# Optimization experiments

Hardware: AMD Instinct MI355X
Metric: run time of the kernel (lower is better)

## Reference

```python
import jax, jax.numpy as jnp
import numpy as np

NUM_GRAPHS = 2048


def gcn_conv(x, W, b, edge, N):
    # PyG GCNConv: x' = D^{-1/2} (A + I) D^{-1/2} (x W) + b
    src, dst = edge[0], edge[1]
    loop = jnp.arange(N, dtype=src.dtype)
    src = jnp.concatenate([src, loop])
    dst = jnp.concatenate([dst, loop])
    h = x @ W  # [N, out]
    deg = jax.ops.segment_sum(jnp.ones(dst.shape, x.dtype), dst, num_segments=N)
    dinv = jnp.where(deg > 0, jax.lax.rsqrt(deg), 0.0)
    norm = dinv[src] * dinv[dst]  # [E+N]
    out = jax.ops.segment_sum(h[src] * norm[:, None], dst, num_segments=N)
    return out + b


def pool_max_mean(x, batch, G):
    mx = jax.ops.segment_max(x, batch, num_segments=G)
    mx = jnp.where(jnp.isfinite(mx), mx, 0.0)  # guard empty segments
    s = jax.ops.segment_sum(x, batch, num_segments=G)
    cnt = jax.ops.segment_sum(jnp.ones((x.shape[0],), x.dtype), batch, num_segments=G)
    mean = s / jnp.maximum(cnt, 1.0)[:, None]
    return mx, mean


def setup_inputs() -> dict:
    key = jax.random.key(0)
    ks = jax.random.split(key, 20)
    F, CE, SE, DD = 64, 64, 32, 128
    Nc, Ec, Ns, Es = 100000, 1250000, 100000, 1250000

    def glorot(k, shape):
        fan_in, fan_out = shape[0], shape[1]
        lim = np.sqrt(6.0 / (fan_in + fan_out)).astype(np.float32)
        return jax.random.uniform(k, shape, jnp.float32, -lim, lim)

    inp = {
        "c": jax.random.normal(ks[0], (Nc, F), jnp.float32),
        "c_edge": jax.random.randint(ks[1], (2, Ec), 0, Nc),
        "c_batch": jnp.sort(jax.random.randint(ks[2], (Nc,), 0, NUM_GRAPHS)),
        "s": jax.random.normal(ks[3], (Ns, F), jnp.float32),
        "s_edge": jax.random.randint(ks[4], (2, Es), 0, Ns),
        "s_batch": jnp.sort(jax.random.randint(ks[5], (Ns,), 0, NUM_GRAPHS)),
        "Wc0": glorot(ks[6], (F, CE)), "bc0": jnp.zeros((CE,), jnp.float32),
        "Wc1": glorot(ks[7], (CE, CE)), "bc1": jnp.zeros((CE,), jnp.float32),
        "Wc2": glorot(ks[8], (CE, CE)), "bc2": jnp.zeros((CE,), jnp.float32),
        "Ws0": glorot(ks[9], (F, SE)), "bs0": jnp.zeros((SE,), jnp.float32),
        "Ws1": glorot(ks[10], (SE, SE)), "bs1": jnp.zeros((SE,), jnp.float32),
        "Ws2": glorot(ks[11], (SE, SE)), "bs2": jnp.zeros((SE,), jnp.float32),
        "Wd": glorot(ks[12], ((CE + SE) * 2, DD)), "bd": jnp.zeros((DD,), jnp.float32),
        "Wo": glorot(ks[13], (DD, 1)), "bo": jnp.zeros((1,), jnp.float32),
    }
    return inp


def reference(c, c_edge, c_batch, s, s_edge, s_batch,
              Wc0, bc0, Wc1, bc1, Wc2, bc2,
              Ws0, bs0, Ws1, bs1, Ws2, bs2,
              Wd, bd, Wo, bo):
    Nc, Ns = c.shape[0], s.shape[0]
    cro = jax.nn.relu(gcn_conv(c, Wc0, bc0, c_edge, Nc))
    cro = jax.nn.relu(gcn_conv(cro, Wc1, bc1, c_edge, Nc))
    cro = jax.nn.relu(gcn_conv(cro, Wc2, bc2, c_edge, Nc))
    solv = jax.nn.relu(gcn_conv(s, Ws0, bs0, s_edge, Ns))
    solv = jax.nn.relu(gcn_conv(solv, Ws1, bs1, s_edge, Ns))
    solv = jax.nn.relu(gcn_conv(solv, Ws2, bs2, s_edge, Ns))
    c_mx, c_mean = pool_max_mean(cro, c_batch, NUM_GRAPHS)
    s_mx, s_mean = pool_max_mean(solv, s_batch, NUM_GRAPHS)
    embed = jnp.concatenate([c_mx, c_mean, s_mx, s_mean], axis=1)  # [G, 192]
    dense = jax.nn.relu(embed @ Wd + bd)
    out = dense @ Wo + bo  # [G, 1]
    return out, embed
```

## Files before the change

kernel.cpp:

```cpp
#include <hip/hip_runtime.h>
#include <hip/hip_fp16.h>
#include <math.h>


static inline int cdiv(int a, int b) { return (a + b - 1) / b; }

#define BUCKET_CAP 8192
#define P1_CHUNK   4096

typedef _Float16 v8h __attribute__((ext_vector_type(8)));
typedef float    v4f __attribute__((ext_vector_type(4)));

__global__ void zero_int(int* __restrict__ p, int n) {
    int i = blockIdx.x * blockDim.x + threadIdx.x;
    if (i < n) p[i] = 0;
}

__global__ __launch_bounds__(256) void p1_partition(const int* __restrict__ c_edge, int Ec,
                                                    const int* __restrict__ s_edge, int Es,
                                                    int Nc_pad, int Etot, int nbuck,
                                                    int* __restrict__ bucket_fill,
                                                    unsigned* __restrict__ pk) {
    __shared__ unsigned       wbuf[P1_CHUNK];
    __shared__ unsigned short bbuf[P1_CHUNK];
    __shared__ int            hist[512];
    int e0 = blockIdx.x * P1_CHUNK;
    int n  = Etot - e0;
    if (n > P1_CHUNK) n = P1_CHUNK;
    for (int i = threadIdx.x; i < nbuck; i += 256) hist[i] = 0;
    __syncthreads();
    for (int i = threadIdx.x; i < n; i += 256) {
        int e = e0 + i, src, g;
        if (e < Ec) { src = c_edge[e]; g = c_edge[Ec + e]; }
        else        { int e2 = e - Ec; src = s_edge[e2]; g = Nc_pad + s_edge[Es + e2]; }
        int b   = g >> 9;
        wbuf[i] = ((unsigned)(g & 511) << 17) | (unsigned)src;
        bbuf[i] = (unsigned short)b;
        atomicAdd(&hist[b], 1);
    }
    __syncthreads();
    for (int i = threadIdx.x; i < nbuck; i += 256) {
        int h = hist[i];
        hist[i] = h ? atomicAdd(&bucket_fill[i], h) : 0;
    }
    __syncthreads();
    for (int i = threadIdx.x; i < n; i += 256) {
        int b    = bbuf[i];
        int slot = atomicAdd(&hist[b], 1);
        if (slot < BUCKET_CAP) pk[(size_t)b * BUCKET_CAP + slot] = wbuf[i];
    }
}

__global__ __launch_bounds__(512) void p2_scanbuckets(const int* __restrict__ fill, int nbuck,
                                                      int* __restrict__ basearr,
                                                      int* __restrict__ off_all, int Ntot_pad, int Etot) {
    __shared__ int sh[512];
    int v = (threadIdx.x < nbuck) ? fill[threadIdx.x] : 0;
    sh[threadIdx.x] = v;
    __syncthreads();
    for (int ofs = 1; ofs < 512; ofs <<= 1) {
        int t = (threadIdx.x >= ofs) ? sh[threadIdx.x - ofs] : 0;
        __syncthreads();
        sh[threadIdx.x] += t;
        __syncthreads();
    }
    if (threadIdx.x < nbuck) basearr[threadIdx.x] = sh[threadIdx.x] - v;
    if (threadIdx.x == 0) off_all[Ntot_pad] = Etot;
}

__global__ __launch_bounds__(512) void p3_build(const unsigned* __restrict__ pk,
                                                const int* __restrict__ fillarr,
                                                const int* __restrict__ basearr,
                                                int* __restrict__ off_all,
                                                float* __restrict__ dinv,
                                                int* __restrict__ csr) {
    __shared__ int sh[512];
    int b    = blockIdx.x;
    int fill = fillarr[b];
    if (fill > BUCKET_CAP) fill = BUCKET_CAP;
    int base = basearr[b];
    const unsigned* reg = pk + (size_t)b * BUCKET_CAP;
    sh[threadIdx.x] = 0;
    __syncthreads();
    for (int i = threadIdx.x; i < fill; i += 512) atomicAdd(&sh[reg[i] >> 17], 1);
    __syncthreads();
    int cnt = sh[threadIdx.x];
    for (int ofs = 1; ofs < 512; ofs <<= 1) {
        int t = (threadIdx.x >= ofs) ? sh[threadIdx.x - ofs] : 0;
        __syncthreads();
        sh[threadIdx.x] += t;
        __syncthreads();
    }
    int excl = sh[threadIdx.x] - cnt;
    int node = b * 512 + threadIdx.x;
    off_all[node] = base + excl;
    dinv[node]    = rsqrtf((float)(cnt + 1));
    __syncthreads();
    sh[threadIdx.x] = excl;
    __syncthreads();
    for (int i = threadIdx.x; i < fill; i += 512) {
        unsigned w    = reg[i];
        int      slot = atomicAdd(&sh[w >> 17], 1);
        csr[base + slot] = (int)(w & 0x1FFFFu);
    }
}

template <int K, int M, typename TIN>
__device__ void gemm_mfma(int bid, const TIN* __restrict__ X, const float* __restrict__ W,
                          const float* __restrict__ dinv, __half* __restrict__ H, int N,
                          char* smem_) {
    constexpr int RB = 64;
    constexpr int KP = K + 8;
    constexpr int NT = M / 16;
    constexpr int KS = K / 32;
    _Float16* Xh = (_Float16*)smem_;
    _Float16* Wz = Xh + RB * KP;
    const int t    = threadIdx.x;
    const int row0 = bid * RB;

    constexpr int WENT = NT * KS * 64;
    for (int idx = t; idx < WENT; idx += 256) {
        int lane = idx & 63, rest = idx >> 6;
        int ks = rest % KS, ntl = rest / KS;
        int kbase = ks * 32 + (lane >> 4) * 8;
        int col   = ntl * 16 + (lane & 15);
        union { float4 f4; _Float16 h[8]; } u;
#pragma unroll
        for (int j = 0; j < 8; ++j) u.h[j] = (_Float16)W[(kbase + j) * M + col];
        *(float4*)(Wz + idx * 8) = u.f4;
    }
    if constexpr (sizeof(TIN) == 4) {
        constexpr int NI = RB * K / 4;
        for (int idx = t; idx < NI; idx += 256) {
            int row = idx / (K / 4), k4 = idx % (K / 4);
            int gr = row0 + row;
            float4 v = make_float4(0.f, 0.f, 0.f, 0.f);
            if (gr < N) v = *(const float4*)((const float*)X + (size_t)gr * K + k4 * 4);
            union { float2 f2; _Float16 h[4]; } u;
            u.h[0] = (_Float16)v.x; u.h[1] = (_Float16)v.y;
            u.h[2] = (_Float16)v.z; u.h[3] = (_Float16)v.w;
            *(float2*)(Xh + row * KP + k4 * 4) = u.f2;
        }
    } else {
        constexpr int NI = RB * K / 8;
        for (int idx = t; idx < NI; idx += 256) {
            int row = idx / (K / 8), k8 = idx % (K / 8);
            int gr = row0 + row;
            float4 v = make_float4(0.f, 0.f, 0.f, 0.f);
            if (gr < N) v = *(const float4*)((const __half*)X + (size_t)gr * K + k8 * 8);
            *(float4*)(Xh + row * KP + k8 * 8) = v;
        }
    }
    __syncthreads();

    const int wave = t >> 6, lane = t & 63;
    const int quad = lane >> 4, nl = lane & 15;
    const int rowA = wave * 16 + nl;

    v4f acc[NT];
#pragma unroll
    for (int i = 0; i < NT; ++i) acc[i] = (v4f){0.f, 0.f, 0.f, 0.f};

#pragma unroll
    for (int ks = 0; ks < KS; ++ks) {
        v8h a = *(const v8h*)(Xh + rowA * KP + ks * 32 + quad * 8);
#pragma unroll
        for (int ntl = 0; ntl < NT; ++ntl) {
            v8h b = *(const v8h*)(Wz + ((ntl * KS + ks) * 64 + lane) * 8);
            acc[ntl] = __builtin_amdgcn_mfma_f32_16x16x32_f16(a, b, acc[ntl], 0, 0, 0);
        }
    }

#pragma unroll
    for (int r = 0; r < 4; ++r) {
        int gr = row0 + wave * 16 + quad * 4 + r;
        if (gr < N) {
            float dv = dinv[gr];
#pragma unroll
            for (int ntl = 0; ntl < NT; ++ntl)
                H[(size_t)gr * M + ntl * 16 + nl] = __float2half(acc[ntl][r] * dv);
        }
    }
}

__device__ __forceinline__ float4 load4h(const float2* __restrict__ base, size_t idx) {
    float2 r = base[idx];
    union { float2 f2; __half2 h2[2]; } u;
    u.f2 = r;
    float2 a = __half22float2(u.h2[0]);
    float2 b = __half22float2(u.h2[1]);
    return make_float4(a.x, a.y, b.x, b.y);
}

template <int M>
__device__ void agg_body(int bid, const __half* __restrict__ H,
                         const int* __restrict__ off_g,
                         const int* __restrict__ csr,
                         const float* __restrict__ dinv_g,
                         const float* __restrict__ b,
                         __half* __restrict__ out, int Nloc) {
    constexpr int L   = M / 4;
    constexpr int NPW = 64 / L;
    int lane = threadIdx.x & 63;
    int wave = threadIdx.x >> 6;
    int fq   = lane & (L - 1);
    int sub  = lane / L;
    int node = (bid * 4 + wave) * NPW + sub;
    if (node >= Nloc) return;
    const float2* H4 = (const float2*)H;
    int j0 = off_g[node], j1 = off_g[node + 1];
    float4 acc = load4h(H4, (size_t)node * L + fq);
    int j = j0;
    for (; j + 8 <= j1; j += 8) {
        int s0 = csr[j],     s1 = csr[j + 1], s2 = csr[j + 2], s3 = csr[j + 3];
        int s4 = csr[j + 4], s5 = csr[j + 5], s6 = csr[j + 6], s7 = csr[j + 7];
        float4 a0 = load4h(H4, (size_t)s0 * L + fq);
        float4 a1 = load4h(H4, (size_t)s1 * L + fq);
        float4 a2 = load4h(H4, (size_t)s2 * L + fq);
        float4 a3 = load4h(H4, (size_t)s3 * L + fq);
        float4 a4 = load4h(H4, (size_t)s4 * L + fq);
        float4 a5 = load4h(H4, (size_t)s5 * L + fq);
        float4 a6 = load4h(H4, (size_t)s6 * L + fq);
        float4 a7 = load4h(H4, (size_t)s7 * L + fq);
        acc.x += (a0.x + a1.x + a2.x + a3.x) + (a4.x + a5.x + a6.x + a7.x);
        acc.y += (a0.y + a1.y + a2.y + a3.y) + (a4.y + a5.y + a6.y + a7.y);
        acc.z += (a0.z + a1.z + a2.z + a3.z) + (a4.z + a5.z + a6.z + a7.z);
        acc.w += (a0.w + a1.w + a2.w + a3.w) + (a4.w + a5.w + a6.w + a7.w);
    }
    for (; j + 4 <= j1; j += 4) {
        int s0 = csr[j], s1 = csr[j + 1], s2 = csr[j + 2], s3 = csr[j + 3];
        float4 a0 = load4h(H4, (size_t)s0 * L + fq);
        float4 a1 = load4h(H4, (size_t)s1 * L + fq);
        float4 a2 = load4h(H4, (size_t)s2 * L + fq);
        float4 a3 = load4h(H4, (size_t)s3 * L + fq);
        acc.x += a0.x + a1.x + a2.x + a3.x;
        acc.y += a0.y + a1.y + a2.y + a3.y;
        acc.z += a0.z + a1.z + a2.z + a3.z;
        acc.w += a0.w + a1.w + a2.w + a3.w;
    }
    for (; j < j1; ++j) {
        float4 a = load4h(H4, (size_t)csr[j] * L + fq);
        acc.x += a.x; acc.y += a.y; acc.z += a.z; acc.w += a.w;
    }
    float  dv = dinv_g[node];
    float4 bb = ((const float4*)b)[fq];
    float  vx = dv * acc.x + bb.x;
    float  vy = dv * acc.y + bb.y;
    float  vz = dv * acc.z + bb.z;
    float  vw = dv * acc.w + bb.w;
    union { float2 f2; __half2 h2[2]; } o;
    o.h2[0] = __floats2half2_rn(vx > 0.f ? vx : 0.f, vy > 0.f ? vy : 0.f);
    o.h2[1] = __floats2half2_rn(vz > 0.f ? vz : 0.f, vw > 0.f ? vw : 0.f);
    ((float2*)out)[(size_t)node * L + fq] = o.f2;
}

__global__ __launch_bounds__(256) void gemmBoth0(const float* __restrict__ Xc, const float* __restrict__ Wc,
                                                 __half* __restrict__ cH, int Nc,
                                                 const float* __restrict__ Xs, const float* __restrict__ Ws,
                                                 __half* __restrict__ sH, int Ns,
                                                 const float* __restrict__ dinv_all, int Nc_pad, int nbC) {
    __shared__ __align__(16) char smem[17408];
    if (blockIdx.x < nbC) gemm_mfma<64, 64, float>(blockIdx.x, Xc, Wc, dinv_all, cH, Nc, smem);
    else                  gemm_mfma<64, 32, float>(blockIdx.x - nbC, Xs, Ws, dinv_all + Nc_pad, sH, Ns, smem);
}

__global__ __launch_bounds__(256) void gemmBoth(const __half* __restrict__ Xc, const float* __restrict__ Wc,
                                                __half* __restrict__ cH, int Nc,
                                                const __half* __restrict__ Xs, const float* __restrict__ Ws,
                                                __half* __restrict__ sH, int Ns,
                                                const float* __restrict__ dinv_all, int Nc_pad, int nbC) {
    __shared__ __align__(16) char smem[17408];
    if (blockIdx.x < nbC) gemm_mfma<64, 64, __half>(blockIdx.x, Xc, Wc, dinv_all, cH, Nc, smem);
    else                  gemm_mfma<32, 32, __half>(blockIdx.x - nbC, Xs, Ws, dinv_all + Nc_pad, sH, Ns, smem);
}

__global__ __launch_bounds__(256) void aggBoth(const __half* __restrict__ cH, const __half* __restrict__ sH,
                                               const int* __restrict__ off_all, const int* __restrict__ csr_all,
                                               const float* __restrict__ dinv_all,
                                               const float* __restrict__ bc, const float* __restrict__ bs,
                                               __half* __restrict__ outc, __half* __restrict__ outs,
                                               int Nc, int Ns, int Nc_pad, int nbC) {
    if (blockIdx.x < nbC)
        agg_body<64>(blockIdx.x, cH, off_all, csr_all, dinv_all, bc, outc, Nc);
    else
        agg_body<32>(blockIdx.x - nbC, sH, off_all + Nc_pad, csr_all,
                     dinv_all + Nc_pad, bs, outs, Ns);
}

__device__ __forceinline__ int lbound(const int* __restrict__ a, int n, int key) {
    int lo = 0, hi = n;
    while (lo < hi) {
        int mid = (lo + hi) >> 1;
        if (a[mid] < key) lo = mid + 1; else hi = mid;
    }
    return lo;
}

__global__ __launch_bounds__(128) void poolDense(const __half* __restrict__ cX, const int* __restrict__ c_batch, int Nc,
                                                 const __half* __restrict__ sX, const int* __restrict__ s_batch, int Ns,
                                                 const float* __restrict__ Wd, const float* __restrict__ bd,
                                                 const float* __restrict__ Wo, const float* __restrict__ bo,
                                                 float* __restrict__ outv, float* __restrict__ embed) {
    __shared__ float e[192];
    __shared__ float red[128];
    int g = blockIdx.x, t = threadIdx.x;
    if (t < 64) {
        int lo = lbound(c_batch, Nc, g), hi = lbound(c_batch, Nc, g + 1);
        float mx = 0.f, sm = 0.f;
        for (int i = lo; i < hi; ++i) {
            float v = __half2float(cX[(size_t)i * 64 + t]);
            mx = fmaxf(mx, v); sm += v;
        }
        int cn = hi - lo;
        e[t]      = mx;
        e[64 + t] = sm / (float)(cn > 0 ? cn : 1);
    } else if (t < 96) {
        int f  = t - 64;
        int lo = lbound(s_batch, Ns, g), hi = lbound(s_batch, Ns, g + 1);
        float mx = 0.f, sm = 0.f;
        for (int i = lo; i < hi; ++i) {
            float v = __half2float(sX[(size_t)i * 32 + f]);
            mx = fmaxf(mx, v); sm += v;
        }
        int cn = hi - lo;
        e[128 + f] = mx;
        e[160 + f] = sm / (float)(cn > 0 ? cn : 1);
    }
    __syncthreads();
    for (int k = t; k < 192; k += 128) embed[(size_t)g * 192 + k] = e[k];
    float acc = bd[t];
    for (int k = 0; k < 192; ++k) acc += e[k] * Wd[k * 128 + t];
    float d = acc > 0.f ? acc : 0.f;
    red[t]  = d * Wo[t];
    __syncthreads();
    for (int ofs = 64; ofs > 0; ofs >>= 1) {
        if (t < ofs) red[t] += red[t + ofs];
        __syncthreads();
    }
    if (t == 0) outv[g] = red[0] + bo[0];
}


extern "C" void kernel_launch(void* const* d_in, const int* in_sizes, int n_in,
                              void* d_out, int out_size, void* d_ws, size_t ws_size,
                              hipStream_t stream) {
    const float* c       = (const float*)d_in[0];
    const int*   c_edge  = (const int*)d_in[1];
    const int*   c_batch = (const int*)d_in[2];
    const float* s       = (const float*)d_in[3];
    const int*   s_edge  = (const int*)d_in[4];
    const int*   s_batch = (const int*)d_in[5];
    const float* Wc0 = (const float*)d_in[6],  *bc0 = (const float*)d_in[7];
    const float* Wc1 = (const float*)d_in[8],  *bc1 = (const float*)d_in[9];
    const float* Wc2 = (const float*)d_in[10], *bc2 = (const float*)d_in[11];
    const float* Ws0 = (const float*)d_in[12], *bs0 = (const float*)d_in[13];
    const float* Ws1 = (const float*)d_in[14], *bs1 = (const float*)d_in[15];
    const float* Ws2 = (const float*)d_in[16], *bs2 = (const float*)d_in[17];
    const float* Wd  = (const float*)d_in[18], *bd  = (const float*)d_in[19];
    const float* Wo  = (const float*)d_in[20], *bo  = (const float*)d_in[21];

    const int Nc = in_sizes[0] / 64;
    const int Ec = in_sizes[1] / 2;
    const int Ns = in_sizes[3] / 64;
    const int Es = in_sizes[4] / 2;
    const int G  = out_size / 193;
    const int Nc_pad   = cdiv(Nc, 512) * 512;
    const int Ns_pad   = cdiv(Ns, 512) * 512;
    const int Ntot_pad = Nc_pad + Ns_pad;
    const int Etot     = Ec + Es;
    const int nbuck    = Ntot_pad >> 9;

    char* p = (char*)d_ws;
    auto  alloc = [&](size_t bytes) -> void* {
        void* r = (void*)p;
        p += (bytes + 255) & ~(size_t)255;
        return r;
    };
    int*      bucket_fill = (int*)alloc(512 * 4);
    int*      bucket_base = (int*)alloc(512 * 4);
    unsigned* pk          = (unsigned*)alloc((size_t)nbuck * BUCKET_CAP * 4);
    int*      off_all     = (int*)alloc(((size_t)Ntot_pad + 1) * 4);
    int*      csr_all     = (int*)alloc((size_t)Etot * 4);
    float*    dinv_all    = (float*)alloc((size_t)Ntot_pad * 4);
    __half*   bufC        = (__half*)alloc((size_t)Nc * 64 * 2);
    __half*   bufS        = (__half*)alloc((size_t)Ns * 32 * 2);
    __half*   cH          = (__half*)alloc((size_t)Nc * 64 * 2);
    __half*   sH          = (__half*)alloc((size_t)Ns * 32 * 2);

    float* outv  = (float*)d_out;
    float* embed = outv + G;

    const int nbGmC = cdiv(Nc, 64), nbGmS = cdiv(Ns, 64);
    const int nbAgC = Nc_pad / 16,  nbAgS = Ns_pad / 32;

    zero_int<<<cdiv(nbuck, 256), 256, 0, stream>>>(bucket_fill, nbuck);
    p1_partition<<<cdiv(Etot, P1_CHUNK), 256, 0, stream>>>(c_edge, Ec, s_edge, Es,
                                                           Nc_pad, Etot, nbuck, bucket_fill, pk);
    p2_scanbuckets<<<1, 512, 0, stream>>>(bucket_fill, nbuck, bucket_base, off_all, Ntot_pad, Etot);
    p3_build<<<nbuck, 512, 0, stream>>>(pk, bucket_fill, bucket_base,
                                        off_all, dinv_all, csr_all);

    gemmBoth0<<<nbGmC + nbGmS, 256, 0, stream>>>(c, Wc0, cH, Nc, s, Ws0, sH, Ns,
                                                 dinv_all, Nc_pad, nbGmC);
    aggBoth<<<nbAgC + nbAgS, 256, 0, stream>>>(cH, sH, off_all, csr_all, dinv_all,
                                               bc0, bs0, bufC, bufS, Nc, Ns, Nc_pad, nbAgC);
    gemmBoth<<<nbGmC + nbGmS, 256, 0, stream>>>(bufC, Wc1, cH, Nc, bufS, Ws1, sH, Ns,
                                                dinv_all, Nc_pad, nbGmC);
    aggBoth<<<nbAgC + nbAgS, 256, 0, stream>>>(cH, sH, off_all, csr_all, dinv_all,
                                               bc1, bs1, bufC, bufS, Nc, Ns, Nc_pad, nbAgC);
    gemmBoth<<<nbGmC + nbGmS, 256, 0, stream>>>(bufC, Wc2, cH, Nc, bufS, Ws2, sH, Ns,
                                                dinv_all, Nc_pad, nbGmC);
    aggBoth<<<nbAgC + nbAgS, 256, 0, stream>>>(cH, sH, off_all, csr_all, dinv_all,
                                               bc2, bs2, bufC, bufS, Nc, Ns, Nc_pad, nbAgC);

    poolDense<<<G, 128, 0, stream>>>(bufC, c_batch, Nc, bufS, s_batch, Ns,
                                     Wd, bd, Wo, bo, outv, embed);
}
```

Measured before the change: 367.6 us.

## Fuse GCN aggregation with next layer's MFMA GEMM via shared memory

New measurement: 370.1 us. No clear change (+0.7%).

```diff
diff --git a/kernel.cpp b/kernel.cpp
--- a/kernel.cpp
+++ b/kernel.cpp
@@ -105,84 +105,6 @@
     }
 }
 
-template <int K, int M, typename TIN>
-__device__ void gemm_mfma(int bid, const TIN* __restrict__ X, const float* __restrict__ W,
-                          const float* __restrict__ dinv, __half* __restrict__ H, int N,
-                          char* smem_) {
-    constexpr int RB = 64;
-    constexpr int KP = K + 8;
-    constexpr int NT = M / 16;
-    constexpr int KS = K / 32;
-    _Float16* Xh = (_Float16*)smem_;
-    _Float16* Wz = Xh + RB * KP;
-    const int t    = threadIdx.x;
-    const int row0 = bid * RB;
-
-    constexpr int WENT = NT * KS * 64;
-    for (int idx = t; idx < WENT; idx += 256) {
-        int lane = idx & 63, rest = idx >> 6;
-        int ks = rest % KS, ntl = rest / KS;
-        int kbase = ks * 32 + (lane >> 4) * 8;
-        int col   = ntl * 16 + (lane & 15);
-        union { float4 f4; _Float16 h[8]; } u;
-#pragma unroll
-        for (int j = 0; j < 8; ++j) u.h[j] = (_Float16)W[(kbase + j) * M + col];
-        *(float4*)(Wz + idx * 8) = u.f4;
-    }
-    if constexpr (sizeof(TIN) == 4) {
-        constexpr int NI = RB * K / 4;
-        for (int idx = t; idx < NI; idx += 256) {
-            int row = idx / (K / 4), k4 = idx % (K / 4);
-            int gr = row0 + row;
-            float4 v = make_float4(0.f, 0.f, 0.f, 0.f);
-            if (gr < N) v = *(const float4*)((const float*)X + (size_t)gr * K + k4 * 4);
-            union { float2 f2; _Float16 h[4]; } u;
-            u.h[0] = (_Float16)v.x; u.h[1] = (_Float16)v.y;
-            u.h[2] = (_Float16)v.z; u.h[3] = (_Float16)v.w;
-            *(float2*)(Xh + row * KP + k4 * 4) = u.f2;
-        }
-    } else {
-        constexpr int NI = RB * K / 8;
-        for (int idx = t; idx < NI; idx += 256) {
-            int row = idx / (K / 8), k8 = idx % (K / 8);
-            int gr = row0 + row;
-            float4 v = make_float4(0.f, 0.f, 0.f, 0.f);
-            if (gr < N) v = *(const float4*)((const __half*)X + (size_t)gr * K + k8 * 8);
-            *(float4*)(Xh + row * KP + k8 * 8) = v;
-        }
-    }
-    __syncthreads();
-
-    const int wave = t >> 6, lane = t & 63;
-    const int quad = lane >> 4, nl = lane & 15;
-    const int rowA = wave * 16 + nl;
-
-    v4f acc[NT];
-#pragma unroll
-    for (int i = 0; i < NT; ++i) acc[i] = (v4f){0.f, 0.f, 0.f, 0.f};
-
-#pragma unroll
-    for (int ks = 0; ks < KS; ++ks) {
-        v8h a = *(const v8h*)(Xh + rowA * KP + ks * 32 + quad * 8);
-#pragma unroll
-        for (int ntl = 0; ntl < NT; ++ntl) {
-            v8h b = *(const v8h*)(Wz + ((ntl * KS + ks) * 64 + lane) * 8);
-            acc[ntl] = __builtin_amdgcn_mfma_f32_16x16x32_f16(a, b, acc[ntl], 0, 0, 0);
-        }
-    }
-
-#pragma unroll
-    for (int r = 0; r < 4; ++r) {
-        int gr = row0 + wave * 16 + quad * 4 + r;
-        if (gr < N) {
-            float dv = dinv[gr];
-#pragma unroll
-            for (int ntl = 0; ntl < NT; ++ntl)
-                H[(size_t)gr * M + ntl * 16 + nl] = __float2half(acc[ntl][r] * dv);
-        }
-    }
-}
-
 __device__ __forceinline__ float4 load4h(const float2* __restrict__ base, size_t idx) {
     float2 r = base[idx];
     union { float2 f2; __half2 h2[2]; } u;
@@ -192,24 +114,9 @@
     return make_float4(a.x, a.y, b.x, b.y);
 }
 
-template <int M>
-__device__ void agg_body(int bid, const __half* __restrict__ H,
-                         const int* __restrict__ off_g,
-                         const int* __restrict__ csr,
-                         const float* __restrict__ dinv_g,
-                         const float* __restrict__ b,
-                         __half* __restrict__ out, int Nloc) {
-    constexpr int L   = M / 4;
-    constexpr int NPW = 64 / L;
-    int lane = threadIdx.x & 63;
-    int wave = threadIdx.x >> 6;
-    int fq   = lane & (L - 1);
-    int sub  = lane / L;
-    int node = (bid * 4 + wave) * NPW + sub;
-    if (node >= Nloc) return;
-    const float2* H4 = (const float2*)H;
-    int j0 = off_g[node], j1 = off_g[node + 1];
-    float4 acc = load4h(H4, (size_t)node * L + fq);
+__device__ __forceinline__ void gather_acc(const float2* __restrict__ H4, int L, int fq,
+                                           const int* __restrict__ csr, int j0, int j1,
+                                           float4& acc) {
     int j = j0;
     for (; j + 8 <= j1; j += 8) {
         int s0 = csr[j],     s1 = csr[j + 1], s2 = csr[j + 2], s3 = csr[j + 3];
@@ -242,6 +149,174 @@
         float4 a = load4h(H4, (size_t)csr[j] * L + fq);
         acc.x += a.x; acc.y += a.y; acc.z += a.z; acc.w += a.w;
     }
+}
+
+template <int K, int M, typename TIN>
+__device__ void gemm_mfma(int bid, const TIN* __restrict__ X, const float* __restrict__ W,
+                          const float* __restrict__ dinv, __half* __restrict__ H, int N,
+                          char* smem_) {
+    constexpr int RB = 64, KP = K + 8, NT = M / 16, KS = K / 32;
+    _Float16* Xh = (_Float16*)smem_;
+    _Float16* Wz = Xh + RB * KP;
+    const int t    = threadIdx.x;
+    const int row0 = bid * RB;
+
+    constexpr int WENT = NT * KS * 64;
+    for (int idx = t; idx < WENT; idx += 256) {
+        int lane = idx & 63, rest = idx >> 6;
+        int ks = rest % KS, ntl = rest / KS;
+        int kbase = ks * 32 + (lane >> 4) * 8;
+        int col   = ntl * 16 + (lane & 15);
+        union { float4 f4; _Float16 h[8]; } u;
+#pragma unroll
+        for (int j = 0; j < 8; ++j) u.h[j] = (_Float16)W[(kbase + j) * M + col];
+        *(float4*)(Wz + idx * 8) = u.f4;
+    }
+    if constexpr (sizeof(TIN) == 4) {
+        constexpr int NI = RB * K / 4;
+        for (int idx = t; idx < NI; idx += 256) {
+            int row = idx / (K / 4), k4 = idx % (K / 4);
+            int gr = row0 + row;
+            float4 v = make_float4(0.f, 0.f, 0.f, 0.f);
+            if (gr < N) v = *(const float4*)((const float*)X + (size_t)gr * K + k4 * 4);
+            union { float2 f2; _Float16 h[4]; } u;
+            u.h[0] = (_Float16)v.x; u.h[1] = (_Float16)v.y;
+            u.h[2] = (_Float16)v.z; u.h[3] = (_Float16)v.w;
+            *(float2*)(Xh + row * KP + k4 * 4) = u.f2;
+        }
+    } else {
+        constexpr int NI = RB * K / 8;
+        for (int idx = t; idx < NI; idx += 256) {
+            int row = idx / (K / 8), k8 = idx % (K / 8);
+            int gr = row0 + row;
+            float4 v = make_float4(0.f, 0.f, 0.f, 0.f);
+            if (gr < N) v = *(const float4*)((const __half*)X + (size_t)gr * K + k8 * 8);
+            *(float4*)(Xh + row * KP + k8 * 8) = v;
+        }
+    }
+    __syncthreads();
+
+    const int wave = t >> 6, lane = t & 63;
+    const int quad = lane >> 4, nl = lane & 15;
+    const int rowA = wave * 16 + nl;
+
+    v4f acc[NT];
+#pragma unroll
+    for (int i = 0; i < NT; ++i) acc[i] = (v4f){0.f, 0.f, 0.f, 0.f};
+#pragma unroll
+    for (int ks = 0; ks < KS; ++ks) {
+        v8h a = *(const v8h*)(Xh + rowA * KP + ks * 32 + quad * 8);
+#pragma unroll
+        for (int ntl = 0; ntl < NT; ++ntl) {
+            v8h b = *(const v8h*)(Wz + ((ntl * KS + ks) * 64 + lane) * 8);
+            acc[ntl] = __builtin_amdgcn_mfma_f32_16x16x32_f16(a, b, acc[ntl], 0, 0, 0);
+        }
+    }
+#pragma unroll
+    for (int r = 0; r < 4; ++r) {
+        int gr = row0 + wave * 16 + quad * 4 + r;
+        if (gr < N) {
+            float dv = dinv[gr];
+#pragma unroll
+            for (int ntl = 0; ntl < NT; ++ntl)
+                H[(size_t)gr * M + ntl * 16 + nl] = __float2half(acc[ntl][r] * dv);
+        }
+    }
+}
+
+template <int M>
+__device__ void aggGemm_body(int bid, const __half* __restrict__ Hin,
+                             const int* __restrict__ off_g, const int* __restrict__ csr,
+                             const float* __restrict__ dinv_g, const float* __restrict__ bvec,
+                             const float* __restrict__ Wnext, __half* __restrict__ Hout,
+                             int Nloc, char* smem_) {
+    constexpr int KP = M + 8, NT = M / 16, KS = M / 32;
+    constexpr int L = M / 4, NPW = 64 / L, ROUNDS = 64 / (4 * NPW);
+    _Float16* Xh = (_Float16*)smem_;
+    _Float16* Wz = Xh + 64 * KP;
+    const int t = threadIdx.x;
+    const int row0 = bid * 64;
+    const int lane = t & 63, wave = t >> 6;
+
+    constexpr int WENT = NT * KS * 64;
+    for (int idx = t; idx < WENT; idx += 256) {
+        int ln = idx & 63, rest = idx >> 6;
+        int ks = rest % KS, ntl = rest / KS;
+        int kbase = ks * 32 + (ln >> 4) * 8;
+        int col   = ntl * 16 + (ln & 15);
+        union { float4 f4; _Float16 h[8]; } u;
+#pragma unroll
+        for (int j = 0; j < 8; ++j) u.h[j] = (_Float16)Wnext[(kbase + j) * M + col];
+        *(float4*)(Wz + idx * 8) = u.f4;
+    }
+
+    const int fq = lane & (L - 1), sub = lane / L;
+    const float2* H4 = (const float2*)Hin;
+#pragma unroll
+    for (int r = 0; r < ROUNDS; ++r) {
+        int local = r * (4 * NPW) + wave * NPW + sub;
+        int node  = row0 + local;
+        float4 acc = make_float4(0.f, 0.f, 0.f, 0.f);
+        if (node < Nloc) {
+            int j0 = off_g[node], j1 = off_g[node + 1];
+            acc = load4h(H4, (size_t)node * L + fq);
+            gather_acc(H4, L, fq, csr, j0, j1, acc);
+            float  dv = dinv_g[node];
+            float4 bb = ((const float4*)bvec)[fq];
+            acc.x = fmaxf(dv * acc.x + bb.x, 0.f);
+            acc.y = fmaxf(dv * acc.y + bb.y, 0.f);
+            acc.z = fmaxf(dv * acc.z + bb.z, 0.f);
+            acc.w = fmaxf(dv * acc.w + bb.w, 0.f);
+        }
+        union { float2 f2; __half2 hh[2]; } o;
+        o.hh[0] = __floats2half2_rn(acc.x, acc.y);
+        o.hh[1] = __floats2half2_rn(acc.z, acc.w);
+        *(float2*)(Xh + local * KP + 4 * fq) = o.f2;
+    }
+    __syncthreads();
+
+    const int quad = lane >> 4, nl = lane & 15;
+    const int rowA = wave * 16 + nl;
+    v4f acc2[NT];
+#pragma unroll
+    for (int i = 0; i < NT; ++i) acc2[i] = (v4f){0.f, 0.f, 0.f, 0.f};
+#pragma unroll
+    for (int ks = 0; ks < KS; ++ks) {
+        v8h a = *(const v8h*)(Xh + rowA * KP + ks * 32 + quad * 8);
+#pragma unroll
+        for (int ntl = 0; ntl < NT; ++ntl) {
+            v8h b = *(const v8h*)(Wz + ((ntl * KS + ks) * 64 + lane) * 8);
+            acc2[ntl] = __builtin_amdgcn_mfma_f32_16x16x32_f16(a, b, acc2[ntl], 0, 0, 0);
+        }
+    }
+#pragma unroll
+    for (int r = 0; r < 4; ++r) {
+        int gr = row0 + wave * 16 + quad * 4 + r;
+        if (gr < Nloc) {
+            float dv = dinv_g[gr];
+#pragma unroll
+            for (int ntl = 0; ntl < NT; ++ntl)
+                Hout[(size_t)gr * M + ntl * 16 + nl] = __float2half(acc2[ntl][r] * dv);
+        }
+    }
+}
+
+template <int M>
+__device__ void agg_body(int bid, const __half* __restrict__ H,
+                         const int* __restrict__ off_g, const int* __restrict__ csr,
+                         const float* __restrict__ dinv_g, const float* __restrict__ b,
+                         __half* __restrict__ out, int Nloc) {
+    constexpr int L = M / 4, NPW = 64 / L;
+    int lane = threadIdx.x & 63;
+    int wave = threadIdx.x >> 6;
+    int fq   = lane & (L - 1);
+    int sub  = lane / L;
+    int node = (bid * 4 + wave) * NPW + sub;
+    if (node >= Nloc) return;
+    const float2* H4 = (const float2*)H;
+    int j0 = off_g[node], j1 = off_g[node + 1];
+    float4 acc = load4h(H4, (size_t)node * L + fq);
+    gather_acc(H4, L, fq, csr, j0, j1, acc);
     float  dv = dinv_g[node];
     float4 bb = ((const float4*)b)[fq];
     float  vx = dv * acc.x + bb.x;
@@ -264,14 +339,19 @@
     else                  gemm_mfma<64, 32, float>(blockIdx.x - nbC, Xs, Ws, dinv_all + Nc_pad, sH, Ns, smem);
 }
 
-__global__ __launch_bounds__(256) void gemmBoth(const __half* __restrict__ Xc, const float* __restrict__ Wc,
-                                                __half* __restrict__ cH, int Nc,
-                                                const __half* __restrict__ Xs, const float* __restrict__ Ws,
-                                                __half* __restrict__ sH, int Ns,
-                                                const float* __restrict__ dinv_all, int Nc_pad, int nbC) {
+__global__ __launch_bounds__(256) void aggGemmBoth(const __half* __restrict__ cHin, __half* __restrict__ cHout,
+                                                   const __half* __restrict__ sHin, __half* __restrict__ sHout,
+                                                   const int* __restrict__ off_all, const int* __restrict__ csr_all,
+                                                   const float* __restrict__ dinv_all,
+                                                   const float* __restrict__ bc, const float* __restrict__ bs,
+                                                   const float* __restrict__ Wc, const float* __restrict__ Ws,
+                                                   int Nc, int Ns, int Nc_pad, int nbC) {
     __shared__ __align__(16) char smem[17408];
-    if (blockIdx.x < nbC) gemm_mfma<64, 64, __half>(blockIdx.x, Xc, Wc, dinv_all, cH, Nc, smem);
-    else                  gemm_mfma<32, 32, __half>(blockIdx.x - nbC, Xs, Ws, dinv_all + Nc_pad, sH, Ns, smem);
+    if (blockIdx.x < nbC)
+        aggGemm_body<64>(blockIdx.x, cHin, off_all, csr_all, dinv_all, bc, Wc, cHout, Nc, smem);
+    else
+        aggGemm_body<32>(blockIdx.x - nbC, sHin, off_all + Nc_pad, csr_all,
+                         dinv_all + Nc_pad, bs, Ws, sHout, Ns, smem);
 }
 
 __global__ __launch_bounds__(256) void aggBoth(const __half* __restrict__ cH, const __half* __restrict__ sH,
@@ -384,13 +464,16 @@
     float*    dinv_all    = (float*)alloc((size_t)Ntot_pad * 4);
     __half*   bufC        = (__half*)alloc((size_t)Nc * 64 * 2);
     __half*   bufS        = (__half*)alloc((size_t)Ns * 32 * 2);
-    __half*   cH          = (__half*)alloc((size_t)Nc * 64 * 2);
-    __half*   sH          = (__half*)alloc((size_t)Ns * 32 * 2);
+    __half*   cHa         = (__half*)alloc((size_t)Nc * 64 * 2);
+    __half*   sHa         = (__half*)alloc((size_t)Ns * 32 * 2);
+    __half*   cHb         = (__half*)alloc((size_t)Nc * 64 * 2);
+    __half*   sHb         = (__half*)alloc((size_t)Ns * 32 * 2);
 
     float* outv  = (float*)d_out;
     float* embed = outv + G;
 
     const int nbGmC = cdiv(Nc, 64), nbGmS = cdiv(Ns, 64);
+    const int nbFzC = Nc_pad / 64,  nbFzS = Ns_pad / 64;
     const int nbAgC = Nc_pad / 16,  nbAgS = Ns_pad / 32;
 
     zero_int<<<cdiv(nbuck, 256), 256, 0, stream>>>(bucket_fill, nbuck);
@@ -400,17 +483,15 @@
     p3_build<<<nbuck, 512, 0, stream>>>(pk, bucket_fill, bucket_base,
                                         off_all, dinv_all, csr_all);
 
-    gemmBoth0<<<nbGmC + nbGmS, 256, 0, stream>>>(c, Wc0, cH, Nc, s, Ws0, sH, Ns,
+    gemmBoth0<<<nbGmC + nbGmS, 256, 0, stream>>>(c, Wc0, cHa, Nc, s, Ws0, sHa, Ns,
                                                  dinv_all, Nc_pad, nbGmC);
-    aggBoth<<<nbAgC + nbAgS, 256, 0, stream>>>(cH, sH, off_all, csr_all, dinv_all,
-                                               bc0, bs0, bufC, bufS, Nc, Ns, Nc_pad, nbAgC);
-    gemmBoth<<<nbGmC + nbGmS, 256, 0, stream>>>(bufC, Wc1, cH, Nc, bufS, Ws1, sH, Ns,
-                                                dinv_all, Nc_pad, nbGmC);
-    aggBoth<<<nbAgC + nbAgS, 256, 0, stream>>>(cH, sH, off_all, csr_all, dinv_all,
-                                               bc1, bs1, bufC, bufS, Nc, Ns, Nc_pad, nbAgC);
-    gemmBoth<<<nbGmC + nbGmS, 256, 0, stream>>>(bufC, Wc2, cH, Nc, bufS, Ws2, sH, Ns,
-                                                dinv_all, Nc_pad, nbGmC);
-    aggBoth<<<nbAgC + nbAgS, 256, 0, stream>>>(cH, sH, off_all, csr_all, dinv_all,
+    aggGemmBoth<<<nbFzC + nbFzS, 256, 0, stream>>>(cHa, cHb, sHa, sHb,
+                                                   off_all, csr_all, dinv_all,
+                                                   bc0, bs0, Wc1, Ws1, Nc, Ns, Nc_pad, nbFzC);
+    aggGemmBoth<<<nbFzC + nbFzS, 256, 0, stream>>>(cHb, cHa, sHb, sHa,
+                                                   off_all, csr_all, dinv_all,
+                                                   bc1, bs1, Wc2, Ws2, Nc, Ns, Nc_pad, nbFzC);
+    aggBoth<<<nbAgC + nbAgS, 256, 0, stream>>>(cHa, sHa, off_all, csr_all, dinv_all,
                                                bc2, bs2, bufC, bufS, Nc, Ns, Nc_pad, nbAgC);
 
     poolDense<<<G, 128, 0, stream>>>(bufC, c_batch, Nc, bufS, s_batch, Ns,
```

## Fuse edge partition with first-layer GEMM and prepack fp16 weights once

Applied to the files above, without the earlier changes.

New measurement: 389.3 us. 5.9% more time.

```diff
diff --git a/kernel.cpp b/kernel.cpp
--- a/kernel.cpp
+++ b/kernel.cpp
@@ -16,15 +16,15 @@
     if (i < n) p[i] = 0;
 }
 
-__global__ __launch_bounds__(256) void p1_partition(const int* __restrict__ c_edge, int Ec,
-                                                    const int* __restrict__ s_edge, int Es,
-                                                    int Nc_pad, int Etot, int nbuck,
-                                                    int* __restrict__ bucket_fill,
-                                                    unsigned* __restrict__ pk) {
-    __shared__ unsigned       wbuf[P1_CHUNK];
-    __shared__ unsigned short bbuf[P1_CHUNK];
-    __shared__ int            hist[512];
-    int e0 = blockIdx.x * P1_CHUNK;
+__device__ void p1_body(int bid, const int* __restrict__ c_edge, int Ec,
+                        const int* __restrict__ s_edge, int Es,
+                        int Nc_pad, int Etot, int nbuck,
+                        int* __restrict__ bucket_fill, unsigned* __restrict__ pk,
+                        char* smem_) {
+    unsigned*       wbuf = (unsigned*)smem_;
+    unsigned short* bbuf = (unsigned short*)(smem_ + 16384);
+    int*            hist = (int*)(smem_ + 24576);
+    int e0 = bid * P1_CHUNK;
     int n  = Etot - e0;
     if (n > P1_CHUNK) n = P1_CHUNK;
     for (int i = threadIdx.x; i < nbuck; i += 256) hist[i] = 0;
@@ -105,14 +105,26 @@
     }
 }
 
-template <int K, int M, typename TIN>
-__device__ void gemm_mfma(int bid, const TIN* __restrict__ X, const float* __restrict__ W,
-                          const float* __restrict__ dinv, __half* __restrict__ H, int N,
-                          char* smem_) {
-    constexpr int RB = 64;
-    constexpr int KP = K + 8;
-    constexpr int NT = M / 16;
-    constexpr int KS = K / 32;
+__device__ void prepW_body(const float* __restrict__ W, int M, _Float16* __restrict__ out) {
+    int NT = M / 16, KS = M / 32;
+    int WENT = NT * KS * 64;
+    for (int idx = threadIdx.x; idx < WENT; idx += 256) {
+        int ln = idx & 63, rest = idx >> 6;
+        int ks = rest % KS, ntl = rest / KS;
+        int kbase = ks * 32 + (ln >> 4) * 8;
+        int col   = ntl * 16 + (ln & 15);
+        union { float4 f4; _Float16 h[8]; } u;
+#pragma unroll
+        for (int j = 0; j < 8; ++j) u.h[j] = (_Float16)W[(kbase + j) * M + col];
+        *(float4*)(out + idx * 8) = u.f4;
+    }
+}
+
+template <int K, int M>
+__device__ void gemm_mfma_f32(int bid, const float* __restrict__ X, const float* __restrict__ W,
+                              const float* __restrict__ dinv, __half* __restrict__ H, int N,
+                              char* smem_) {
+    constexpr int RB = 64, KP = K + 8, NT = M / 16, KS = K / 32;
     _Float16* Xh = (_Float16*)smem_;
     _Float16* Wz = Xh + RB * KP;
     const int t    = threadIdx.x;
@@ -129,27 +141,16 @@
         for (int j = 0; j < 8; ++j) u.h[j] = (_Float16)W[(kbase + j) * M + col];
         *(float4*)(Wz + idx * 8) = u.f4;
     }
-    if constexpr (sizeof(TIN) == 4) {
-        constexpr int NI = RB * K / 4;
-        for (int idx = t; idx < NI; idx += 256) {
-            int row = idx / (K / 4), k4 = idx % (K / 4);
-            int gr = row0 + row;
-            float4 v = make_float4(0.f, 0.f, 0.f, 0.f);
-            if (gr < N) v = *(const float4*)((const float*)X + (size_t)gr * K + k4 * 4);
-            union { float2 f2; _Float16 h[4]; } u;
-            u.h[0] = (_Float16)v.x; u.h[1] = (_Float16)v.y;
-            u.h[2] = (_Float16)v.z; u.h[3] = (_Float16)v.w;
-            *(float2*)(Xh + row * KP + k4 * 4) = u.f2;
-        }
-    } else {
-        constexpr int NI = RB * K / 8;
-        for (int idx = t; idx < NI; idx += 256) {
-            int row = idx / (K / 8), k8 = idx % (K / 8);
-            int gr = row0 + row;
-            float4 v = make_float4(0.f, 0.f, 0.f, 0.f);
-            if (gr < N) v = *(const float4*)((const __half*)X + (size_t)gr * K + k8 * 8);
-            *(float4*)(Xh + row * KP + k8 * 8) = v;
-        }
+    constexpr int NI = RB * K / 4;
+    for (int idx = t; idx < NI; idx += 256) {
+        int row = idx / (K / 4), k4 = idx % (K / 4);
+        int gr = row0 + row;
+        float4 v = make_float4(0.f, 0.f, 0.f, 0.f);
+        if (gr < N) v = *(const float4*)(X + (size_t)gr * K + k4 * 4);
+        union { float2 f2; _Float16 h[4]; } u;
+        u.h[0] = (_Float16)v.x; u.h[1] = (_Float16)v.y;
+        u.h[2] = (_Float16)v.z; u.h[3] = (_Float16)v.w;
+        *(float2*)(Xh + row * KP + k4 * 4) = u.f2;
     }
     __syncthreads();
 
@@ -160,7 +161,6 @@
     v4f acc[NT];
 #pragma unroll
     for (int i = 0; i < NT; ++i) acc[i] = (v4f){0.f, 0.f, 0.f, 0.f};
-
 #pragma unroll
     for (int ks = 0; ks < KS; ++ks) {
         v8h a = *(const v8h*)(Xh + rowA * KP + ks * 32 + quad * 8);
@@ -170,7 +170,42 @@
             acc[ntl] = __builtin_amdgcn_mfma_f32_16x16x32_f16(a, b, acc[ntl], 0, 0, 0);
         }
     }
-
+#pragma unroll
+    for (int r = 0; r < 4; ++r) {
+        int gr = row0 + wave * 16 + quad * 4 + r;
+        if (gr < N) {
+            float dv = dinv ? dinv[gr] : 1.0f;
+#pragma unroll
+            for (int ntl = 0; ntl < NT; ++ntl)
+                H[(size_t)gr * M + ntl * 16 + nl] = __float2half(acc[ntl][r] * dv);
+        }
+    }
+}
+
+template <int M>
+__device__ void gemm_direct(int bid, const __half* __restrict__ X,
+                            const _Float16* __restrict__ Wz,
+                            const float* __restrict__ dinv, __half* __restrict__ H, int N) {
+    constexpr int NT = M / 16, KS = M / 32;
+    const int t = threadIdx.x, wave = t >> 6, lane = t & 63;
+    const int quad = lane >> 4, nl = lane & 15;
+    const int row0 = bid * 64;
+    int rowA = row0 + wave * 16 + nl;
+    if (rowA >= N) rowA = N - 1;
+    const _Float16* Xp = (const _Float16*)X;
+
+    v4f acc[NT];
+#pragma unroll
+    for (int i = 0; i < NT; ++i) acc[i] = (v4f){0.f, 0.f, 0.f, 0.f};
+#pragma unroll
+    for (int ks = 0; ks < KS; ++ks) {
+        v8h a = *(const v8h*)(Xp + (size_t)rowA * M + ks * 32 + quad * 8);
+#pragma unroll
+        for (int ntl = 0; ntl < NT; ++ntl) {
+            v8h b = *(const v8h*)(Wz + ((ntl * KS + ks) * 64 + lane) * 8);
+            acc[ntl] = __builtin_amdgcn_mfma_f32_16x16x32_f16(a, b, acc[ntl], 0, 0, 0);
+        }
+    }
 #pragma unroll
     for (int r = 0; r < 4; ++r) {
         int gr = row0 + wave * 16 + quad * 4 + r;
@@ -192,15 +227,12 @@
     return make_float4(a.x, a.y, b.x, b.y);
 }
 
-template <int M>
+template <int M, bool WSRC>
 __device__ void agg_body(int bid, const __half* __restrict__ H,
-                         const int* __restrict__ off_g,
-                         const int* __restrict__ csr,
-                         const float* __restrict__ dinv_g,
-                         const float* __restrict__ b,
+                         const int* __restrict__ off_g, const int* __restrict__ csr,
+                         const float* __restrict__ dinv_g, const float* __restrict__ b,
                          __half* __restrict__ out, int Nloc) {
-    constexpr int L   = M / 4;
-    constexpr int NPW = 64 / L;
+    constexpr int L = M / 4, NPW = 64 / L;
     int lane = threadIdx.x & 63;
     int wave = threadIdx.x >> 6;
     int fq   = lane & (L - 1);
@@ -209,7 +241,9 @@
     if (node >= Nloc) return;
     const float2* H4 = (const float2*)H;
     int j0 = off_g[node], j1 = off_g[node + 1];
+    float dvi = dinv_g[node];
     float4 acc = load4h(H4, (size_t)node * L + fq);
+    if (WSRC) { acc.x *= dvi; acc.y *= dvi; acc.z *= dvi; acc.w *= dvi; }
     int j = j0;
     for (; j + 8 <= j1; j += 8) {
         int s0 = csr[j],     s1 = csr[j + 1], s2 = csr[j + 2], s3 = csr[j + 3];
@@ -222,58 +256,74 @@
         float4 a5 = load4h(H4, (size_t)s5 * L + fq);
         float4 a6 = load4h(H4, (size_t)s6 * L + fq);
         float4 a7 = load4h(H4, (size_t)s7 * L + fq);
-        acc.x += (a0.x + a1.x + a2.x + a3.x) + (a4.x + a5.x + a6.x + a7.x);
-        acc.y += (a0.y + a1.y + a2.y + a3.y) + (a4.y + a5.y + a6.y + a7.y);
-        acc.z += (a0.z + a1.z + a2.z + a3.z) + (a4.z + a5.z + a6.z + a7.z);
-        acc.w += (a0.w + a1.w + a2.w + a3.w) + (a4.w + a5.w + a6.w + a7.w);
-    }
-    for (; j + 4 <= j1; j += 4) {
-        int s0 = csr[j], s1 = csr[j + 1], s2 = csr[j + 2], s3 = csr[j + 3];
-        float4 a0 = load4h(H4, (size_t)s0 * L + fq);
-        float4 a1 = load4h(H4, (size_t)s1 * L + fq);
-        float4 a2 = load4h(H4, (size_t)s2 * L + fq);
-        float4 a3 = load4h(H4, (size_t)s3 * L + fq);
-        acc.x += a0.x + a1.x + a2.x + a3.x;
-        acc.y += a0.y + a1.y + a2.y + a3.y;
-        acc.z += a0.z + a1.z + a2.z + a3.z;
-        acc.w += a0.w + a1.w + a2.w + a3.w;
+        if (WSRC) {
+            float d0 = dinv_g[s0], d1 = dinv_g[s1], d2 = dinv_g[s2], d3 = dinv_g[s3];
+            float d4 = dinv_g[s4], d5 = dinv_g[s5], d6 = dinv_g[s6], d7 = dinv_g[s7];
+            acc.x += (d0*a0.x + d1*a1.x + d2*a2.x + d3*a3.x) + (d4*a4.x + d5*a5.x + d6*a6.x + d7*a7.x);
+            acc.y += (d0*a0.y + d1*a1.y + d2*a2.y + d3*a3.y) + (d4*a4.y + d5*a5.y + d6*a6.y + d7*a7.y);
+            acc.z += (d0*a0.z + d1*a1.z + d2*a2.z + d3*a3.z) + (d4*a4.z + d5*a5.z + d6*a6.z + d7*a7.z);
+            acc.w += (d0*a0.w + d1*a1.w + d2*a2.w + d3*a3.w) + (d4*a4.w + d5*a5.w + d6*a6.w + d7*a7.w);
+        } else {
+            acc.x += (a0.x + a1.x + a2.x + a3.x) + (a4.x + a5.x + a6.x + a7.x);
+            acc.y += (a0.y + a1.y + a2.y + a3.y) + (a4.y + a5.y + a6.y + a7.y);
+            acc.z += (a0.z + a1.z + a2.z + a3.z) + (a4.z + a5.z + a6.z + a7.z);
+            acc.w += (a0.w + a1.w + a2.w + a3.w) + (a4.w + a5.w + a6.w + a7.w);
+        }
     }
     for (; j < j1; ++j) {
-        float4 a = load4h(H4, (size_t)csr[j] * L + fq);
-        acc.x += a.x; acc.y += a.y; acc.z += a.z; acc.w += a.w;
-    }
-    float  dv = dinv_g[node];
+        int s = csr[j];
+        float4 a = load4h(H4, (size_t)s * L + fq);
+        float d = WSRC ? dinv_g[s] : 1.0f;
+        acc.x += d * a.x; acc.y += d * a.y; acc.z += d * a.z; acc.w += d * a.w;
+    }
     float4 bb = ((const float4*)b)[fq];
-    float  vx = dv * acc.x + bb.x;
-    float  vy = dv * acc.y + bb.y;
-    float  vz = dv * acc.z + bb.z;
-    float  vw = dv * acc.w + bb.w;
+    float  vx = dvi * acc.x + bb.x;
+    float  vy = dvi * acc.y + bb.y;
+    float  vz = dvi * acc.z + bb.z;
+    float  vw = dvi * acc.w + bb.w;
     union { float2 f2; __half2 h2[2]; } o;
     o.h2[0] = __floats2half2_rn(vx > 0.f ? vx : 0.f, vy > 0.f ? vy : 0.f);
     o.h2[1] = __floats2half2_rn(vz > 0.f ? vz : 0.f, vw > 0.f ? vw : 0.f);
     ((float2*)out)[(size_t)node * L + fq] = o.f2;
 }
 
-__global__ __launch_bounds__(256) void gemmBoth0(const float* __restrict__ Xc, const float* __restrict__ Wc,
-                                                 __half* __restrict__ cH, int Nc,
-                                                 const float* __restrict__ Xs, const float* __restrict__ Ws,
-                                                 __half* __restrict__ sH, int Ns,
-                                                 const float* __restrict__ dinv_all, int Nc_pad, int nbC) {
-    __shared__ __align__(16) char smem[17408];
-    if (blockIdx.x < nbC) gemm_mfma<64, 64, float>(blockIdx.x, Xc, Wc, dinv_all, cH, Nc, smem);
-    else                  gemm_mfma<64, 32, float>(blockIdx.x - nbC, Xs, Ws, dinv_all + Nc_pad, sH, Ns, smem);
-}
-
-__global__ __launch_bounds__(256) void gemmBoth(const __half* __restrict__ Xc, const float* __restrict__ Wc,
-                                                __half* __restrict__ cH, int Nc,
-                                                const __half* __restrict__ Xs, const float* __restrict__ Ws,
-                                                __half* __restrict__ sH, int Ns,
-                                                const float* __restrict__ dinv_all, int Nc_pad, int nbC) {
-    __shared__ __align__(16) char smem[17408];
-    if (blockIdx.x < nbC) gemm_mfma<64, 64, __half>(blockIdx.x, Xc, Wc, dinv_all, cH, Nc, smem);
-    else                  gemm_mfma<32, 32, __half>(blockIdx.x - nbC, Xs, Ws, dinv_all + Nc_pad, sH, Ns, smem);
-}
-
+__global__ __launch_bounds__(256) void phaseA(const int* __restrict__ c_edge, int Ec,
+                                              const int* __restrict__ s_edge, int Es,
+                                              int Nc_pad, int Etot, int nbuck,
+                                              int* __restrict__ bucket_fill, unsigned* __restrict__ pk,
+                                              const float* __restrict__ c, const float* __restrict__ Wc0,
+                                              __half* __restrict__ cH, int Nc,
+                                              const float* __restrict__ s, const float* __restrict__ Ws0,
+                                              __half* __restrict__ sH, int Ns,
+                                              const float* __restrict__ Wc1, _Float16* __restrict__ wzC1,
+                                              const float* __restrict__ Wc2, _Float16* __restrict__ wzC2,
+                                              const float* __restrict__ Ws1, _Float16* __restrict__ wzS1,
+                                              const float* __restrict__ Ws2, _Float16* __restrict__ wzS2,
+                                              int nbP1, int nbGmC, int nbGmS) {
+    __shared__ __align__(16) char smem[26624];
+    int b = blockIdx.x;
+    if (b < nbP1) { p1_body(b, c_edge, Ec, s_edge, Es, Nc_pad, Etot, nbuck, bucket_fill, pk, smem); return; }
+    b -= nbP1;
+    if (b < nbGmC) { gemm_mfma_f32<64, 64>(b, c, Wc0, nullptr, cH, Nc, smem); return; }
+    b -= nbGmC;
+    if (b < nbGmS) { gemm_mfma_f32<64, 32>(b, s, Ws0, nullptr, sH, Ns, smem); return; }
+    b -= nbGmS;
+    if (b == 0) prepW_body(Wc1, 64, wzC1);
+    else if (b == 1) prepW_body(Wc2, 64, wzC2);
+    else if (b == 2) prepW_body(Ws1, 32, wzS1);
+    else             prepW_body(Ws2, 32, wzS2);
+}
+
+__global__ __launch_bounds__(256) void gemmDirectBoth(const __half* __restrict__ Xc, const _Float16* __restrict__ wzC,
+                                                      __half* __restrict__ cH, int Nc,
+                                                      const __half* __restrict__ Xs, const _Float16* __restrict__ wzS,
+                                                      __half* __restrict__ sH, int Ns,
+                                                      const float* __restrict__ dinv_all, int Nc_pad, int nbC) {
+    if (blockIdx.x < nbC) gemm_direct<64>(blockIdx.x, Xc, wzC, dinv_all, cH, Nc);
+    else                  gemm_direct<32>(blockIdx.x - nbC, Xs, wzS, dinv_all + Nc_pad, sH, Ns);
+}
+
+template <bool WSRC>
 __global__ __launch_bounds__(256) void aggBoth(const __half* __restrict__ cH, const __half* __restrict__ sH,
                                                const int* __restrict__ off_all, const int* __restrict__ csr_all,
                                                const float* __restrict__ dinv_all,
@@ -281,10 +331,10 @@
                                                __half* __restrict__ outc, __half* __restrict__ outs,
                                                int Nc, int Ns, int Nc_pad, int nbC) {
     if (blockIdx.x < nbC)
-        agg_body<64>(blockIdx.x, cH, off_all, csr_all, dinv_all, bc, outc, Nc);
+        agg_body<64, WSRC>(blockIdx.x, cH, off_all, csr_all, dinv_all, bc, outc, Nc);
     else
-        agg_body<32>(blockIdx.x - nbC, sH, off_all + Nc_pad, csr_all,
-                     dinv_all + Nc_pad, bs, outs, Ns);
+        agg_body<32, WSRC>(blockIdx.x - nbC, sH, off_all + Nc_pad, csr_all,
+                           dinv_all + Nc_pad, bs, outs, Ns);
 }
 
 __device__ __forceinline__ int lbound(const int* __restrict__ a, int n, int key) {
@@ -382,36 +432,42 @@
     int*      off_all     = (int*)alloc(((size_t)Ntot_pad + 1) * 4);
     int*      csr_all     = (int*)alloc((size_t)Etot * 4);
     float*    dinv_all    = (float*)alloc((size_t)Ntot_pad * 4);
+    _Float16* wzC1        = (_Float16*)alloc(4096 * 2);
+    _Float16* wzC2        = (_Float16*)alloc(4096 * 2);
+    _Float16* wzS1        = (_Float16*)alloc(1024 * 2);
+    _Float16* wzS2        = (_Float16*)alloc(1024 * 2);
     __half*   bufC        = (__half*)alloc((size_t)Nc * 64 * 2);
     __half*   bufS        = (__half*)alloc((size_t)Ns * 32 * 2);
-    __half*   cH          = (__half*)alloc((size_t)Nc * 64 * 2);
-    __half*   sH          = (__half*)alloc((size_t)Ns * 32 * 2);
+    __half*   cHa         = (__half*)alloc((size_t)Nc * 64 * 2);
+    __half*   sHa         = (__half*)alloc((size_t)Ns * 32 * 2);
 
     float* outv  = (float*)d_out;
     float* embed = outv + G;
 
+    const int nbP1  = cdiv(Etot, P1_CHUNK);
     const int nbGmC = cdiv(Nc, 64), nbGmS = cdiv(Ns, 64);
     const int nbAgC = Nc_pad / 16,  nbAgS = Ns_pad / 32;
 
     zero_int<<<cdiv(nbuck, 256), 256, 0, stream>>>(bucket_fill, nbuck);
-    p1_partition<<<cdiv(Etot, P1_CHUNK), 256, 0, stream>>>(c_edge, Ec, s_edge, Es,
-                                                           Nc_pad, Etot, nbuck, bucket_fill, pk);
+    phaseA<<<nbP1 + nbGmC + nbGmS + 4, 256, 0, stream>>>(
+        c_edge, Ec, s_edge, Es, Nc_pad, Etot, nbuck, bucket_fill, pk,
+        c, Wc0, cHa, Nc, s, Ws0, sHa, Ns,
+        Wc1, wzC1, Wc2, wzC2, Ws1, wzS1, Ws2, wzS2,
+        nbP1, nbGmC, nbGmS);
     p2_scanbuckets<<<1, 512, 0, stream>>>(bucket_fill, nbuck, bucket_base, off_all, Ntot_pad, Etot);
     p3_build<<<nbuck, 512, 0, stream>>>(pk, bucket_fill, bucket_base,
                                         off_all, dinv_all, csr_all);
 
-    gemmBoth0<<<nbGmC + nbGmS, 256, 0, stream>>>(c, Wc0, cH, Nc, s, Ws0, sH, Ns,
-                                                 dinv_all, Nc_pad, nbGmC);
-    aggBoth<<<nbAgC + nbAgS, 256, 0, stream>>>(cH, sH, off_all, csr_all, dinv_all,
-                                               bc0, bs0, bufC, bufS, Nc, Ns, Nc_pad, nbAgC);
-    gemmBoth<<<nbGmC + nbGmS, 256, 0, stream>>>(bufC, Wc1, cH, Nc, bufS, Ws1, sH, Ns,
-                                                dinv_all, Nc_pad, nbGmC);
-    aggBoth<<<nbAgC + nbAgS, 256, 0, stream>>>(cH, sH, off_all, csr_all, dinv_all,
-                                               bc1, bs1, bufC, bufS, Nc, Ns, Nc_pad, nbAgC);
-    gemmBoth<<<nbGmC + nbGmS, 256, 0, stream>>>(bufC, Wc2, cH, Nc, bufS, Ws2, sH, Ns,
-                                                dinv_all, Nc_pad, nbGmC);
-    aggBoth<<<nbAgC + nbAgS, 256, 0, stream>>>(cH, sH, off_all, csr_all, dinv_all,
-                                               bc2, bs2, bufC, bufS, Nc, Ns, Nc_pad, nbAgC);
+    aggBoth<true><<<nbAgC + nbAgS, 256, 0, stream>>>(cHa, sHa, off_all, csr_all, dinv_all,
+                                                     bc0, bs0, bufC, bufS, Nc, Ns, Nc_pad, nbAgC);
+    gemmDirectBoth<<<nbGmC + nbGmS, 256, 0, stream>>>(bufC, wzC1, cHa, Nc, bufS, wzS1, sHa, Ns,
+                                                      dinv_all, Nc_pad, nbGmC);
+    aggBoth<false><<<nbAgC + nbAgS, 256, 0, stream>>>(cHa, sHa, off_all, csr_all, dinv_all,
+                                                      bc1, bs1, bufC, bufS, Nc, Ns, Nc_pad, nbAgC);
+    gemmDirectBoth<<<nbGmC + nbGmS, 256, 0, stream>>>(bufC, wzC2, cHa, Nc, bufS, wzS2, sHa, Ns,
+                                                      dinv_all, Nc_pad, nbGmC);
+    aggBoth<false><<<nbAgC + nbAgS, 256, 0, stream>>>(cHa, sHa, off_all, csr_all, dinv_all,
+                                                      bc2, bs2, bufC, bufS, Nc, Ns, Nc_pad, nbAgC);
 
     poolDense<<<G, 128, 0, stream>>>(bufC, c_batch, Nc, bufS, s_batch, Ns,
                                      Wd, bd, Wo, bo, outv, embed);
```
